# Optimization experiments

Measured on AMD Instinct MI355X. Metric: run time of the kernel, lower is better.

## Reference

```python
import jax, jax.numpy as jnp
import numpy as np

DIM = 2048
N_HEADS = 16
N_KV_HEADS = 4
HEAD_DIM = DIM // N_HEADS  # 128
N_REP = N_HEADS // N_KV_HEADS
MAX_SEQ_LEN = 4096
SEQLEN = 4096


def setup_inputs() -> dict:
    key = jax.random.key(0)
    ks = jax.random.split(key, 6)
    x = jax.random.normal(ks[0], (1, SEQLEN, DIM), dtype=jnp.float32)
    # rotary frequencies, llama-style theta=10000
    inv_freq = 1.0 / (10000.0 ** (np.arange(0, HEAD_DIM, 2, dtype=np.float32) / HEAD_DIM))
    t = np.arange(SEQLEN, dtype=np.float32)
    ang = np.outer(t, inv_freq)  # [S, head_dim/2]
    freqs_cos = jnp.asarray(np.cos(ang))
    freqs_sin = jnp.asarray(np.sin(ang))
    # additive causal mask [S, S]
    mask = jnp.where(jnp.tril(jnp.ones((SEQLEN, SEQLEN), dtype=bool)), 0.0, -1e9).astype(jnp.float32)
    sc = 0.02
    wq = jax.random.normal(ks[1], (DIM, N_HEADS * HEAD_DIM), dtype=jnp.float32) * sc
    wk = jax.random.normal(ks[2], (DIM, N_KV_HEADS * HEAD_DIM), dtype=jnp.float32) * sc
    wv = jax.random.normal(ks[3], (DIM, N_KV_HEADS * HEAD_DIM), dtype=jnp.float32) * sc
    wo = jax.random.normal(ks[4], (N_HEADS * HEAD_DIM, DIM), dtype=jnp.float32) * sc
    return {"x": x, "start_pos": 0, "freqs_cos": freqs_cos, "freqs_sin": freqs_sin,
            "mask": mask, "wq": wq, "wk": wk, "wv": wv, "wo": wo}


def _rope(x, cos, sin):
    # x: [b, s, h, d]; cos/sin: [s, d/2]; consecutive pairs form complex numbers
    b, s, h, d = x.shape
    xr = x.astype(jnp.float32).reshape(b, s, h, d // 2, 2)
    x1, x2 = xr[..., 0], xr[..., 1]
    c = cos[None, :, None, :]
    sn = sin[None, :, None, :]
    o1 = x1 * c - x2 * sn
    o2 = x1 * sn + x2 * c
    return jnp.stack([o1, o2], axis=-1).reshape(b, s, h, d).astype(x.dtype)


def reference(x, start_pos, freqs_cos, freqs_sin, mask, wq, wk, wv, wo):
    bsz, seqlen, _ = x.shape
    xq = (x @ wq).reshape(bsz, seqlen, N_HEADS, HEAD_DIM)
    xk = (x @ wk).reshape(bsz, seqlen, N_KV_HEADS, HEAD_DIM)
    xv = (x @ wv).reshape(bsz, seqlen, N_KV_HEADS, HEAD_DIM)
    xq = _rope(xq, freqs_cos, freqs_sin)
    xk = _rope(xk, freqs_cos, freqs_sin)
    # KV-cache append (cache is zeros before this call)
    cache_k = jnp.zeros((1, MAX_SEQ_LEN, N_KV_HEADS, HEAD_DIM), dtype=xk.dtype)
    cache_v = jnp.zeros((1, MAX_SEQ_LEN, N_KV_HEADS, HEAD_DIM), dtype=xv.dtype)
    cache_k = jax.lax.dynamic_update_slice(cache_k, xk, (0, start_pos, 0, 0))
    cache_v = jax.lax.dynamic_update_slice(cache_v, xv, (0, start_pos, 0, 0))
    keys = cache_k[:bsz, : start_pos + seqlen]    # [b, T, kvh, d]
    values = cache_v[:bsz, : start_pos + seqlen]
    # GQA repeat to full head count
    keys = jnp.repeat(keys, N_REP, axis=2)
    values = jnp.repeat(values, N_REP, axis=2)
    scale = 1.0 / jnp.sqrt(jnp.float32(HEAD_DIM))
    scores = jnp.einsum('bshd,bthd->bhst', xq, keys) * scale  # [b, h, s, T]
    scores = scores + mask[None, None, :, :]
    probs = jax.nn.softmax(scores.astype(jnp.float32), axis=-1).astype(xq.dtype)
    out = jnp.einsum('bhst,bthd->bshd', probs, values).reshape(bsz, seqlen, -1)
    return out @ wo
```

## Files before the change

### kernel.cpp

```cpp
#include <hip/hip_runtime.h>
#include <hip/hip_bf16.h>
#include <stdint.h>

#define SEQ 4096
#define DIM 2048
#define NH 16
#define NKV 4
#define HD 128
#define KVLD 1024


using frag8 = __attribute__((ext_vector_type(8))) short;
using f32x4 = __attribute__((ext_vector_type(4))) float;

union VecU { ushort u[8]; uint4 v; };

__device__ __forceinline__ float bf2f(ushort u) {
    union { uint32_t u; float f; } v; v.u = ((uint32_t)u) << 16; return v.f;
}
__device__ __forceinline__ ushort f2bf(float f) {
    union { float f; uint32_t u; } v; v.f = f;
    uint32_t r = v.u + 0x7fffu + ((v.u >> 16) & 1u);
    return (ushort)(r >> 16);
}

__device__ __forceinline__ void glds16(const void* g, void* l) {
    __builtin_amdgcn_global_load_lds(
        (const __attribute__((address_space(1))) void*)g,
        (__attribute__((address_space(3))) void*)l, 16, 0, 0);
}

__global__ __launch_bounds__(256) void cvt_kernel(
    const float* __restrict__ src, ushort* __restrict__ dst)
{
    size_t i = ((size_t)blockIdx.x * 256 + threadIdx.x) * 8;
    float4 f0 = *(const float4*)&src[i];
    float4 f1 = *(const float4*)&src[i + 4];
    VecU t;
    t.u[0] = f2bf(f0.x); t.u[1] = f2bf(f0.y); t.u[2] = f2bf(f0.z); t.u[3] = f2bf(f0.w);
    t.u[4] = f2bf(f1.x); t.u[5] = f2bf(f1.y); t.u[6] = f2bf(f1.z); t.u[7] = f2bf(f1.w);
    *(uint4*)&dst[i] = t.v;
}

__global__ __launch_bounds__(256) void convT_kernel(
    const float* __restrict__ src, ushort* __restrict__ dst, int K, int N)
{
    __shared__ ushort T[32][36];
    int r  = threadIdx.x >> 3;
    int c4 = (threadIdx.x & 7) * 4;
    int bk = blockIdx.y * 32, bn = blockIdx.x * 32;
    float4 v = *(const float4*)&src[(size_t)(bk + r) * N + bn + c4];
    T[r][c4]     = f2bf(v.x); T[r][c4 + 1] = f2bf(v.y);
    T[r][c4 + 2] = f2bf(v.z); T[r][c4 + 3] = f2bf(v.w);
    __syncthreads();
    ushort4 o;
    o.x = T[c4][r]; o.y = T[c4 + 1][r]; o.z = T[c4 + 2][r]; o.w = T[c4 + 3][r];
    *(ushort4*)&dst[(size_t)(bn + r) * K + bk + c4] = o;
}

__global__ __launch_bounds__(256) void vtrans_kernel(
    const ushort* __restrict__ src, ushort* __restrict__ dst)
{
    __shared__ ushort T[32][36];
    int r  = threadIdx.x >> 3;
    int c4 = (threadIdx.x & 7) * 4;
    int bt = blockIdx.y * 32, bd = blockIdx.x * 32;
    ushort4 v = *(const ushort4*)&src[(size_t)(bt + r) * KVLD + 512 + bd + c4];
    T[r][c4] = v.x; T[r][c4 + 1] = v.y; T[r][c4 + 2] = v.z; T[r][c4 + 3] = v.w;
    __syncthreads();
    ushort4 o;
    o.x = T[c4][r]; o.y = T[c4 + 1][r]; o.z = T[c4 + 2][r]; o.w = T[c4 + 3][r];
    *(ushort4*)&dst[(size_t)(bd + r) * SEQ + bt + c4] = o;
}

template <int CF>
__global__ __launch_bounds__(256) void gemm_tn(
    const ushort* __restrict__ A, const ushort* __restrict__ BT,
    void* __restrict__ C, int M, int N, int K)
{
    __shared__ ushort As[128 * 32];
    __shared__ ushort Bs[128 * 32];

    const int tid  = threadIdx.x;
    const int lane = tid & 63;
    const int wave = tid >> 6;
    const int bm   = blockIdx.y * 128;
    const int bn   = blockIdx.x * 128;
    const int wm   = (wave >> 1) * 64;
    const int wn   = (wave & 1) * 64;
    const int quad = lane >> 4;
    const int t16  = lane & 15;
    const int kg   = quad ^ ((t16 >> 1) & 3);

    f32x4 acc[4][4] = {};

    for (int k0 = 0; k0 < K; k0 += 32) {
        #pragma unroll
        for (int it = 0; it < 2; ++it) {
            int gid = it * 256 + tid;
            int r   = gid >> 2;
            int cs  = (gid & 3) ^ ((gid >> 3) & 3);
            glds16(&A[(size_t)(bm + r) * K + k0 + cs * 8],
                   &As[(it * 256 + wave * 64) * 8]);
            glds16(&BT[(size_t)(bn + r) * K + k0 + cs * 8],
                   &Bs[(it * 256 + wave * 64) * 8]);
        }
        __syncthreads();

        frag8 af[4], bf[4];
        #pragma unroll
        for (int i = 0; i < 4; ++i)
            af[i] = *(const frag8*)&As[(wm + i * 16 + t16) * 32 + kg * 8];
        #pragma unroll
        for (int j = 0; j < 4; ++j)
            bf[j] = *(const frag8*)&Bs[(wn + j * 16 + t16) * 32 + kg * 8];
        #pragma unroll
        for (int i = 0; i < 4; ++i)
            #pragma unroll
            for (int j = 0; j < 4; ++j)
                acc[i][j] = __builtin_amdgcn_mfma_f32_16x16x32_bf16(
                    af[i], bf[j], acc[i][j], 0, 0, 0);
        __syncthreads();
    }

    #pragma unroll
    for (int i = 0; i < 4; ++i)
        #pragma unroll
        for (int j = 0; j < 4; ++j)
            #pragma unroll
            for (int r = 0; r < 4; ++r) {
                int row = bm + wm + i * 16 + quad * 4 + r;
                int col = bn + wn + j * 16 + t16;
                if (CF) ((float*)C)[(size_t)row * N + col] = acc[i][j][r];
                else    ((ushort*)C)[(size_t)row * N + col] = f2bf(acc[i][j][r]);
            }
}

__global__ __launch_bounds__(256) void gemm_qkv(
    const ushort* __restrict__ A, const ushort* __restrict__ BT,
    ushort* __restrict__ Cq, ushort* __restrict__ Ckv)
{
    const int K = DIM;
    __shared__ ushort As[128 * 32];
    __shared__ ushort Bs[128 * 32];

    const int tid  = threadIdx.x;
    const int lane = tid & 63;
    const int wave = tid >> 6;
    const int bm   = blockIdx.y * 128;
    const int bn   = blockIdx.x * 128;
    const int wm   = (wave >> 1) * 64;
    const int wn   = (wave & 1) * 64;
    const int quad = lane >> 4;
    const int t16  = lane & 15;
    const int kg   = quad ^ ((t16 >> 1) & 3);

    f32x4 acc[4][4] = {};

    for (int k0 = 0; k0 < K; k0 += 32) {
        #pragma unroll
        for (int it = 0; it < 2; ++it) {
            int gid = it * 256 + tid;
            int r   = gid >> 2;
            int cs  = (gid & 3) ^ ((gid >> 3) & 3);
            glds16(&A[(size_t)(bm + r) * K + k0 + cs * 8],
                   &As[(it * 256 + wave * 64) * 8]);
            glds16(&BT[(size_t)(bn + r) * K + k0 + cs * 8],
                   &Bs[(it * 256 + wave * 64) * 8]);
        }
        __syncthreads();

        frag8 af[4], bf[4];
        #pragma unroll
        for (int i = 0; i < 4; ++i)
            af[i] = *(const frag8*)&As[(wm + i * 16 + t16) * 32 + kg * 8];
        #pragma unroll
        for (int j = 0; j < 4; ++j)
            bf[j] = *(const frag8*)&Bs[(wn + j * 16 + t16) * 32 + kg * 8];
        #pragma unroll
        for (int i = 0; i < 4; ++i)
            #pragma unroll
            for (int j = 0; j < 4; ++j)
                acc[i][j] = __builtin_amdgcn_mfma_f32_16x16x32_bf16(
                    af[i], bf[j], acc[i][j], 0, 0, 0);
        __syncthreads();
    }

    ushort* C;
    int ldc, cb;
    if (bn < 2048) { C = Cq;  ldc = DIM;  cb = 0; }
    else           { C = Ckv; ldc = KVLD; cb = 2048; }

    #pragma unroll
    for (int i = 0; i < 4; ++i)
        #pragma unroll
        for (int j = 0; j < 4; ++j)
            #pragma unroll
            for (int r = 0; r < 4; ++r) {
                int row = bm + wm + i * 16 + quad * 4 + r;
                int col = bn + wn + j * 16 + t16;
                C[(size_t)row * ldc + (col - cb)] = f2bf(acc[i][j][r]);
            }
}

__global__ void rope_kernel(ushort* __restrict__ X, const float* __restrict__ Cos,
                            const float* __restrict__ Sin, int log2nh, int strideT,
                            float oscale)
{
    int idx = blockIdx.x * blockDim.x + threadIdx.x;
    int p = idx & 63;
    int h = (idx >> 6) & ((1 << log2nh) - 1);
    int t = idx >> (6 + log2nh);
    size_t base = (size_t)t * strideT + (size_t)h * 128 + 2 * p;
    ushort2 xv = *(ushort2*)&X[base];
    float x1 = bf2f(xv.x), x2 = bf2f(xv.y);
    float c = Cos[t * 64 + p], s = Sin[t * 64 + p];
    ushort2 ov;
    ov.x = f2bf((x1 * c - x2 * s) * oscale);
    ov.y = f2bf((x1 * s + x2 * c) * oscale);
    *(ushort2*)&X[base] = ov;
}

__global__ __launch_bounds__(256) void attn_kernel(
    const ushort* __restrict__ Q, const ushort* __restrict__ Kb,
    const ushort* __restrict__ VT, ushort* __restrict__ O)
{
    __shared__ ushort Ks[64][136];
    __shared__ ushort Vt[128][72];
    __shared__ ushort Sp[4][16][72];

    const int tid  = threadIdx.x;
    const int lane = tid & 63;
    const int wave = tid >> 6;
    const int quad = lane >> 4;
    const int t16  = lane & 15;
    const int h    = blockIdx.x;
    const int kvh  = h >> 2;

    frag8 vONE;
    #pragma unroll
    for (int i = 0; i < 8; ++i) vONE[i] = (short)0x3F80;

    const int qt = 63 - (int)blockIdx.y;
    const int q0 = qt * 64;
    const int qwave = q0 + wave * 16;
    const int qmaxw = qwave + 15;

    frag8 aQ[4];
    #pragma unroll
    for (int kk = 0; kk < 4; ++kk)
        aQ[kk] = *(const frag8*)&Q[(size_t)(qwave + t16) * DIM + h * HD + kk * 32 + quad * 8];

    f32x4 o[8] = {};
    f32x4 o9 = {0.f, 0.f, 0.f, 0.f};
    float mrow[4];
    #pragma unroll
    for (int r = 0; r < 4; ++r) mrow[r] = -30000.f;

    for (int t0 = 0; t0 <= q0 + 63; t0 += 64) {
        #pragma unroll
        for (int it = 0; it < 4; ++it) {
            int idx = tid + it * 256;
            int tt  = idx >> 4;
            int c   = (idx & 15) * 8;
            *(uint4*)&Ks[tt][c] =
                *(const uint4*)&Kb[(size_t)(t0 + tt) * KVLD + kvh * HD + c];
        }
        #pragma unroll
        for (int it = 0; it < 4; ++it) {
            int idx = tid + it * 256;
            int d   = idx >> 3;
            int tq  = (idx & 7) * 8;
            *(uint4*)&Vt[d][tq] =
                *(const uint4*)&VT[(size_t)(kvh * HD + d) * SEQ + t0 + tq];
        }
        __syncthreads();

        const bool hi = (t0 + 32 <= qmaxw);
        {
            f32x4 s0 = {0.f, 0.f, 0.f, 0.f};
            f32x4 s1 = {0.f, 0.f, 0.f, 0.f};
            f32x4 s2 = {0.f, 0.f, 0.f, 0.f};
            f32x4 s3 = {0.f, 0.f, 0.f, 0.f};
            __builtin_amdgcn_s_setprio(1);
            #pragma unroll
            for (int kk = 0; kk < 4; ++kk) {
                frag8 b0 = *(const frag8*)&Ks[2 * t16][kk * 32 + quad * 8];
                frag8 b1 = *(const frag8*)&Ks[2 * t16 + 1][kk * 32 + quad * 8];
                s0 = __builtin_amdgcn_mfma_f32_16x16x32_bf16(aQ[kk], b0, s0, 0, 0, 0);
                s1 = __builtin_amdgcn_mfma_f32_16x16x32_bf16(aQ[kk], b1, s1, 0, 0, 0);
            }
            if (hi) {
                #pragma unroll
                for (int kk = 0; kk < 4; ++kk) {
                    frag8 b2 = *(const frag8*)&Ks[32 + 2 * t16][kk * 32 + quad * 8];
                    frag8 b3 = *(const frag8*)&Ks[33 + 2 * t16][kk * 32 + quad * 8];
                    s2 = __builtin_amdgcn_mfma_f32_16x16x32_bf16(aQ[kk], b2, s2, 0, 0, 0);
                    s3 = __builtin_amdgcn_mfma_f32_16x16x32_bf16(aQ[kk], b3, s3, 0, 0, 0);
                }
            }
            __builtin_amdgcn_s_setprio(0);

            const bool mLo = (t0 + 31 > qwave);
            const bool mHi = (t0 + 63 > qwave);
            float v[4][4];
            float mnew[4];
            bool trig = false;
            #pragma unroll
            for (int r = 0; r < 4; ++r) {
                int q = qwave + quad * 4 + r;
                float v0 = s0[r];
                float v1 = s1[r];
                float v2 = hi ? s2[r] : -30000.f;
                float v3 = hi ? s3[r] : -30000.f;
                if (mLo) {
                    if (t0 + 2 * t16 > q)      v0 = -30000.f;
                    if (t0 + 2 * t16 + 1 > q)  v1 = -30000.f;
                }
                if (hi && mHi) {
                    if (t0 + 32 + 2 * t16 > q) v2 = -30000.f;
                    if (t0 + 33 + 2 * t16 > q) v3 = -30000.f;
                }
                float rm = fmaxf(fmaxf(v0, v1), fmaxf(v2, v3));
                rm = fmaxf(rm, __shfl_xor(rm, 1));
                rm = fmaxf(rm, __shfl_xor(rm, 2));
                rm = fmaxf(rm, __shfl_xor(rm, 4));
                rm = fmaxf(rm, __shfl_xor(rm, 8));
                mnew[r] = fmaxf(mrow[r], rm);
                trig |= (rm > mrow[r] + 8.f);
                v[r][0] = v0; v[r][1] = v1; v[r][2] = v2; v[r][3] = v3;
            }
            if (__any(trig)) {
                #pragma unroll
                for (int r = 0; r < 4; ++r) {
                    float alpha = __expf(mrow[r] - mnew[r]);
                    mrow[r] = mnew[r];
                    #pragma unroll
                    for (int j = 0; j < 8; ++j) o[j][r] *= alpha;
                    o9[r] *= alpha;
                }
            }
            #pragma unroll
            for (int r = 0; r < 4; ++r) {
                float e0 = __expf(v[r][0] - mrow[r]);
                float e1 = __expf(v[r][1] - mrow[r]);
                uint pv = (uint)f2bf(e0) | ((uint)f2bf(e1) << 16);
                *(uint*)&Sp[wave][quad * 4 + r][2 * t16] = pv;
                if (hi) {
                    float e2 = __expf(v[r][2] - mrow[r]);
                    float e3 = __expf(v[r][3] - mrow[r]);
                    uint ph = (uint)f2bf(e2) | ((uint)f2bf(e3) << 16);
                    *(uint*)&Sp[wave][quad * 4 + r][32 + 2 * t16] = ph;
                }
            }

            frag8 aP0 = *(const frag8*)&Sp[wave][t16][quad * 8];
            __builtin_amdgcn_s_setprio(1);
            #pragma unroll
            for (int j = 0; j < 8; ++j) {
                frag8 bV = *(const frag8*)&Vt[j * 16 + t16][quad * 8];
                o[j] = __builtin_amdgcn_mfma_f32_16x16x32_bf16(aP0, bV, o[j], 0, 0, 0);
            }
            o9 = __builtin_amdgcn_mfma_f32_16x16x32_bf16(aP0, vONE, o9, 0, 0, 0);
            if (hi) {
                frag8 aP1 = *(const frag8*)&Sp[wave][t16][32 + quad * 8];
                #pragma unroll
                for (int j = 0; j < 8; ++j) {
                    frag8 bV = *(const frag8*)&Vt[j * 16 + t16][32 + quad * 8];
                    o[j] = __builtin_amdgcn_mfma_f32_16x16x32_bf16(aP1, bV, o[j], 0, 0, 0);
                }
                o9 = __builtin_amdgcn_mfma_f32_16x16x32_bf16(aP1, vONE, o9, 0, 0, 0);
            }
            __builtin_amdgcn_s_setprio(0);
        }
        __syncthreads();
    }

    #pragma unroll
    for (int r = 0; r < 4; ++r) {
        float inv = 1.f / fmaxf(o9[r], 1e-20f);
        int row = qwave + quad * 4 + r;
        #pragma unroll
        for (int j = 0; j < 8; ++j)
            O[(size_t)row * DIM + h * HD + j * 16 + t16] = f2bf(o[j][r] * inv);
    }
}

extern "C" void kernel_launch(void* const* d_in, const int* in_sizes, int n_in,
                              void* d_out, int out_size, void* d_ws, size_t ws_size,
                              hipStream_t stream)
{
    const float* x  = (const float*)d_in[0];
    const float* fc = (const float*)d_in[2];
    const float* fs = (const float*)d_in[3];
    const float* wq = (const float*)d_in[5];
    const float* wk = (const float*)d_in[6];
    const float* wv = (const float*)d_in[7];
    const float* wo = (const float*)d_in[8];

    ushort* Qb  = (ushort*)d_ws;
    ushort* KVb = Qb + (size_t)SEQ * DIM;
    ushort* Ab  = KVb + (size_t)SEQ * KVLD;
    ushort* WqT = Ab;
    ushort* KVT = Ab + (size_t)DIM * DIM;
    ushort* WoT = KVb;

    ushort* Xb = (ushort*)d_out;
    ushort* VT = Xb + (size_t)SEQ * DIM;

    dim3 blk(256);

    cvt_kernel<<<(SEQ * DIM) / 2048, blk, 0, stream>>>(x, Xb);
    convT_kernel<<<dim3(DIM / 32, DIM / 32), blk, 0, stream>>>(wq, WqT, DIM, DIM);
    convT_kernel<<<dim3(512 / 32, DIM / 32), blk, 0, stream>>>(wk, KVT, DIM, 512);
    convT_kernel<<<dim3(512 / 32, DIM / 32), blk, 0, stream>>>(
        wv, KVT + (size_t)512 * DIM, DIM, 512);

    gemm_qkv<<<dim3(3072 / 128, SEQ / 128), blk, 0, stream>>>(Xb, Ab, Qb, KVb);

    rope_kernel<<<(SEQ * NH * 64) / 256, blk, 0, stream>>>(
        Qb, fc, fs, 4, DIM, 0.08838834764831845f);
    rope_kernel<<<(SEQ * NKV * 64) / 256, blk, 0, stream>>>(
        KVb, fc, fs, 2, KVLD, 1.0f);

    vtrans_kernel<<<dim3(512 / 32, SEQ / 32), blk, 0, stream>>>(KVb, VT);

    attn_kernel<<<dim3(NH, 64), blk, 0, stream>>>(Qb, KVb, VT, Ab);

    convT_kernel<<<dim3(DIM / 32, DIM / 32), blk, 0, stream>>>(wo, WoT, DIM, DIM);
    gemm_tn<1><<<dim3(DIM / 128, SEQ / 128), blk, 0, stream>>>(Ab, WoT, d_out, SEQ, DIM, DIM);
}
```

Baseline: 452.8 us.

## Process two query heads per attention block to reuse K/V tiles

Each attention workgroup now handles two query heads that share one KV head, so every K and V tile staged in shared memory serves twice the MFMA work and the grid is halved. The softmax is restructured to compute exponentials optimistically against the previous running max and to recompute only when a row max rises by more than a threshold. The running max now starts at zero instead of a large negative value. Launch bounds request two blocks per CU. The cost is roughly doubled accumulator and Q-fragment registers, which may cause spills or lower occupancy, and fewer blocks to spread across the CUs.

```diff
diff --git a/kernel.cpp b/kernel.cpp
--- a/kernel.cpp
+++ b/kernel.cpp
@@ -221,21 +221,23 @@
     *(ushort2*)&X[base] = ov;
 }
 
-__global__ __launch_bounds__(256) void attn_kernel(
+__global__ __launch_bounds__(256, 2) void attn_kernel(
     const ushort* __restrict__ Q, const ushort* __restrict__ Kb,
     const ushort* __restrict__ VT, ushort* __restrict__ O)
 {
     __shared__ ushort Ks[64][136];
     __shared__ ushort Vt[128][72];
-    __shared__ ushort Sp[4][16][72];
+    __shared__ ushort Sp[4][32][72];
 
     const int tid  = threadIdx.x;
     const int lane = tid & 63;
     const int wave = tid >> 6;
     const int quad = lane >> 4;
     const int t16  = lane & 15;
-    const int h    = blockIdx.x;
-    const int kvh  = h >> 2;
+    const int hp   = blockIdx.x;
+    const int hA   = 2 * hp;
+    const int hB   = 2 * hp + 1;
+    const int kvh  = hp >> 1;
 
     frag8 vONE;
     #pragma unroll
@@ -246,16 +248,18 @@
     const int qwave = q0 + wave * 16;
     const int qmaxw = qwave + 15;
 
-    frag8 aQ[4];
+    frag8 aQA[4], aQB[4];
     #pragma unroll
-    for (int kk = 0; kk < 4; ++kk)
-        aQ[kk] = *(const frag8*)&Q[(size_t)(qwave + t16) * DIM + h * HD + kk * 32 + quad * 8];
-
-    f32x4 o[8] = {};
-    f32x4 o9 = {0.f, 0.f, 0.f, 0.f};
-    float mrow[4];
-    #pragma unroll
-    for (int r = 0; r < 4; ++r) mrow[r] = -30000.f;
+    for (int kk = 0; kk < 4; ++kk) {
+        aQA[kk] = *(const frag8*)&Q[(size_t)(qwave + t16) * DIM + hA * HD + kk * 32 + quad * 8];
+        aQB[kk] = *(const frag8*)&Q[(size_t)(qwave + t16) * DIM + hB * HD + kk * 32 + quad * 8];
+    }
+
+    f32x4 oA[8] = {}, oB[8] = {};
+    f32x4 o9A = {0.f, 0.f, 0.f, 0.f};
+    f32x4 o9B = {0.f, 0.f, 0.f, 0.f};
+    float mA[4] = {0.f, 0.f, 0.f, 0.f};
+    float mB[4] = {0.f, 0.f, 0.f, 0.f};
 
     for (int t0 = 0; t0 <= q0 + 63; t0 += 64) {
         #pragma unroll
@@ -277,112 +281,169 @@
         __syncthreads();
 
         const bool hi = (t0 + 32 <= qmaxw);
-        {
-            f32x4 s0 = {0.f, 0.f, 0.f, 0.f};
-            f32x4 s1 = {0.f, 0.f, 0.f, 0.f};
-            f32x4 s2 = {0.f, 0.f, 0.f, 0.f};
-            f32x4 s3 = {0.f, 0.f, 0.f, 0.f};
-            __builtin_amdgcn_s_setprio(1);
+
+        f32x4 sA0 = {0.f,0.f,0.f,0.f}, sA1 = {0.f,0.f,0.f,0.f};
+        f32x4 sA2 = {0.f,0.f,0.f,0.f}, sA3 = {0.f,0.f,0.f,0.f};
+        f32x4 sB0 = {0.f,0.f,0.f,0.f}, sB1 = {0.f,0.f,0.f,0.f};
+        f32x4 sB2 = {0.f,0.f,0.f,0.f}, sB3 = {0.f,0.f,0.f,0.f};
+
+        __builtin_amdgcn_s_setprio(1);
+        #pragma unroll
+        for (int kk = 0; kk < 4; ++kk) {
+            frag8 b0 = *(const frag8*)&Ks[2 * t16][kk * 32 + quad * 8];
+            frag8 b1 = *(const frag8*)&Ks[2 * t16 + 1][kk * 32 + quad * 8];
+            sA0 = __builtin_amdgcn_mfma_f32_16x16x32_bf16(aQA[kk], b0, sA0, 0, 0, 0);
+            sB0 = __builtin_amdgcn_mfma_f32_16x16x32_bf16(aQB[kk], b0, sB0, 0, 0, 0);
+            sA1 = __builtin_amdgcn_mfma_f32_16x16x32_bf16(aQA[kk], b1, sA1, 0, 0, 0);
+            sB1 = __builtin_amdgcn_mfma_f32_16x16x32_bf16(aQB[kk], b1, sB1, 0, 0, 0);
+        }
+        if (hi) {
             #pragma unroll
             for (int kk = 0; kk < 4; ++kk) {
-                frag8 b0 = *(const frag8*)&Ks[2 * t16][kk * 32 + quad * 8];
-                frag8 b1 = *(const frag8*)&Ks[2 * t16 + 1][kk * 32 + quad * 8];
-                s0 = __builtin_amdgcn_mfma_f32_16x16x32_bf16(aQ[kk], b0, s0, 0, 0, 0);
-                s1 = __builtin_amdgcn_mfma_f32_16x16x32_bf16(aQ[kk], b1, s1, 0, 0, 0);
-            }
+                frag8 b2 = *(const frag8*)&Ks[32 + 2 * t16][kk * 32 + quad * 8];
+                frag8 b3 = *(const frag8*)&Ks[33 + 2 * t16][kk * 32 + quad * 8];
+                sA2 = __builtin_amdgcn_mfma_f32_16x16x32_bf16(aQA[kk], b2, sA2, 0, 0, 0);
+                sB2 = __builtin_amdgcn_mfma_f32_16x16x32_bf16(aQB[kk], b2, sB2, 0, 0, 0);
+                sA3 = __builtin_amdgcn_mfma_f32_16x16x32_bf16(aQA[kk], b3, sA3, 0, 0, 0);
+                sB3 = __builtin_amdgcn_mfma_f32_16x16x32_bf16(aQB[kk], b3, sB3, 0, 0, 0);
+            }
+        }
+        __builtin_amdgcn_s_setprio(0);
+
+        const bool mLo = (t0 + 31 > qwave);
+        const bool mHi = (t0 + 63 > qwave);
+
+        bool trig = false;
+        #pragma unroll
+        for (int r = 0; r < 4; ++r) {
+            int q = qwave + quad * 4 + r;
+            bool x0 = mLo && (t0 + 2 * t16 > q);
+            bool x1 = mLo && (t0 + 2 * t16 + 1 > q);
+            bool x2 = mHi && (t0 + 32 + 2 * t16 > q);
+            bool x3 = mHi && (t0 + 33 + 2 * t16 > q);
+            float vA0 = x0 ? -30000.f : sA0[r];
+            float vA1 = x1 ? -30000.f : sA1[r];
+            float vA2 = (hi && !x2) ? sA2[r] : -30000.f;
+            float vA3 = (hi && !x3) ? sA3[r] : -30000.f;
+            float vB0 = x0 ? -30000.f : sB0[r];
+            float vB1 = x1 ? -30000.f : sB1[r];
+            float vB2 = (hi && !x2) ? sB2[r] : -30000.f;
+            float vB3 = (hi && !x3) ? sB3[r] : -30000.f;
+            float lmA = fmaxf(fmaxf(vA0, vA1), fmaxf(vA2, vA3));
+            float lmB = fmaxf(fmaxf(vB0, vB1), fmaxf(vB2, vB3));
+            trig |= (lmA > mA[r] + 8.f) | (lmB > mB[r] + 8.f);
+            float eA0 = __expf(vA0 - mA[r]);
+            float eA1 = __expf(vA1 - mA[r]);
+            float eB0 = __expf(vB0 - mB[r]);
+            float eB1 = __expf(vB1 - mB[r]);
+            *(uint*)&Sp[wave][quad * 4 + r][2 * t16] =
+                (uint)f2bf(eA0) | ((uint)f2bf(eA1) << 16);
+            *(uint*)&Sp[wave][16 + quad * 4 + r][2 * t16] =
+                (uint)f2bf(eB0) | ((uint)f2bf(eB1) << 16);
             if (hi) {
-                #pragma unroll
-                for (int kk = 0; kk < 4; ++kk) {
-                    frag8 b2 = *(const frag8*)&Ks[32 + 2 * t16][kk * 32 + quad * 8];
-                    frag8 b3 = *(const frag8*)&Ks[33 + 2 * t16][kk * 32 + quad * 8];
-                    s2 = __builtin_amdgcn_mfma_f32_16x16x32_bf16(aQ[kk], b2, s2, 0, 0, 0);
-                    s3 = __builtin_amdgcn_mfma_f32_16x16x32_bf16(aQ[kk], b3, s3, 0, 0, 0);
-                }
-            }
-            __builtin_amdgcn_s_setprio(0);
-
-            const bool mLo = (t0 + 31 > qwave);
-            const bool mHi = (t0 + 63 > qwave);
-            float v[4][4];
-            float mnew[4];
-            bool trig = false;
+                float eA2 = __expf(vA2 - mA[r]);
+                float eA3 = __expf(vA3 - mA[r]);
+                float eB2 = __expf(vB2 - mB[r]);
+                float eB3 = __expf(vB3 - mB[r]);
+                *(uint*)&Sp[wave][quad * 4 + r][32 + 2 * t16] =
+                    (uint)f2bf(eA2) | ((uint)f2bf(eA3) << 16);
+                *(uint*)&Sp[wave][16 + quad * 4 + r][32 + 2 * t16] =
+                    (uint)f2bf(eB2) | ((uint)f2bf(eB3) << 16);
+            }
+        }
+
+        if (__any(trig)) {
             #pragma unroll
             for (int r = 0; r < 4; ++r) {
                 int q = qwave + quad * 4 + r;
-                float v0 = s0[r];
-                float v1 = s1[r];
-                float v2 = hi ? s2[r] : -30000.f;
-                float v3 = hi ? s3[r] : -30000.f;
-                if (mLo) {
-                    if (t0 + 2 * t16 > q)      v0 = -30000.f;
-                    if (t0 + 2 * t16 + 1 > q)  v1 = -30000.f;
+                bool x0 = mLo && (t0 + 2 * t16 > q);
+                bool x1 = mLo && (t0 + 2 * t16 + 1 > q);
+                bool x2 = mHi && (t0 + 32 + 2 * t16 > q);
+                bool x3 = mHi && (t0 + 33 + 2 * t16 > q);
+                float vA0 = x0 ? -30000.f : sA0[r];
+                float vA1 = x1 ? -30000.f : sA1[r];
+                float vA2 = (hi && !x2) ? sA2[r] : -30000.f;
+                float vA3 = (hi && !x3) ? sA3[r] : -30000.f;
+                float vB0 = x0 ? -30000.f : sB0[r];
+                float vB1 = x1 ? -30000.f : sB1[r];
+                float vB2 = (hi && !x2) ? sB2[r] : -30000.f;
+                float vB3 = (hi && !x3) ? sB3[r] : -30000.f;
+                float rmA = fmaxf(fmaxf(vA0, vA1), fmaxf(vA2, vA3));
+                float rmB = fmaxf(fmaxf(vB0, vB1), fmaxf(vB2, vB3));
+                rmA = fmaxf(rmA, __shfl_xor(rmA, 1));
+                rmA = fmaxf(rmA, __shfl_xor(rmA, 2));
+                rmA = fmaxf(rmA, __shfl_xor(rmA, 4));
+                rmA = fmaxf(rmA, __shfl_xor(rmA, 8));
+                rmB = fmaxf(rmB, __shfl_xor(rmB, 1));
+                rmB = fmaxf(rmB, __shfl_xor(rmB, 2));
+                rmB = fmaxf(rmB, __shfl_xor(rmB, 4));
+                rmB = fmaxf(rmB, __shfl_xor(rmB, 8));
+                float mnA = fmaxf(mA[r], rmA);
+                float mnB = fmaxf(mB[r], rmB);
+                float alA = __expf(mA[r] - mnA);
+                float alB = __expf(mB[r] - mnB);
+                #pragma unroll
+                for (int j = 0; j < 8; ++j) { oA[j][r] *= alA; oB[j][r] *= alB; }
+                o9A[r] *= alA; o9B[r] *= alB;
+                mA[r] = mnA; mB[r] = mnB;
+                float eA0 = __expf(vA0 - mnA);
+                float eA1 = __expf(vA1 - mnA);
+                float eB0 = __expf(vB0 - mnB);
+                float eB1 = __expf(vB1 - mnB);
+                *(uint*)&Sp[wave][quad * 4 + r][2 * t16] =
+                    (uint)f2bf(eA0) | ((uint)f2bf(eA1) << 16);
+                *(uint*)&Sp[wave][16 + quad * 4 + r][2 * t16] =
+                    (uint)f2bf(eB0) | ((uint)f2bf(eB1) << 16);
+                if (hi) {
+                    float eA2 = __expf(vA2 - mnA);
+                    float eA3 = __expf(vA3 - mnA);
+                    float eB2 = __expf(vB2 - mnB);
+                    float eB3 = __expf(vB3 - mnB);
+                    *(uint*)&Sp[wave][quad * 4 + r][32 + 2 * t16] =
+                        (uint)f2bf(eA2) | ((uint)f2bf(eA3) << 16);
+                    *(uint*)&Sp[wave][16 + quad * 4 + r][32 + 2 * t16] =
+                        (uint)f2bf(eB2) | ((uint)f2bf(eB3) << 16);
                 }
-                if (hi && mHi) {
-                    if (t0 + 32 + 2 * t16 > q) v2 = -30000.f;
-                    if (t0 + 33 + 2 * t16 > q) v3 = -30000.f;
-                }
-                float rm = fmaxf(fmaxf(v0, v1), fmaxf(v2, v3));
-                rm = fmaxf(rm, __shfl_xor(rm, 1));
-                rm = fmaxf(rm, __shfl_xor(rm, 2));
-                rm = fmaxf(rm, __shfl_xor(rm, 4));
-                rm = fmaxf(rm, __shfl_xor(rm, 8));
-                mnew[r] = fmaxf(mrow[r], rm);
-                trig |= (rm > mrow[r] + 8.f);
-                v[r][0] = v0; v[r][1] = v1; v[r][2] = v2; v[r][3] = v3;
-            }
-            if (__any(trig)) {
-                #pragma unroll
-                for (int r = 0; r < 4; ++r) {
-                    float alpha = __expf(mrow[r] - mnew[r]);
-                    mrow[r] = mnew[r];
-                    #pragma unroll
-                    for (int j = 0; j < 8; ++j) o[j][r] *= alpha;
-                    o9[r] *= alpha;
-                }
-            }
-            #pragma unroll
-            for (int r = 0; r < 4; ++r) {
-                float e0 = __expf(v[r][0] - mrow[r]);
-                float e1 = __expf(v[r][1] - mrow[r]);
-                uint pv = (uint)f2bf(e0) | ((uint)f2bf(e1) << 16);
-                *(uint*)&Sp[wave][quad * 4 + r][2 * t16] = pv;
-                if (hi) {
-                    float e2 = __expf(v[r][2] - mrow[r]);
-                    float e3 = __expf(v[r][3] - mrow[r]);
-                    uint ph = (uint)f2bf(e2) | ((uint)f2bf(e3) << 16);
-                    *(uint*)&Sp[wave][quad * 4 + r][32 + 2 * t16] = ph;
-                }
-            }
-
-            frag8 aP0 = *(const frag8*)&Sp[wave][t16][quad * 8];
-            __builtin_amdgcn_s_setprio(1);
+            }
+        }
+
+        frag8 aPA0 = *(const frag8*)&Sp[wave][t16][quad * 8];
+        frag8 aPB0 = *(const frag8*)&Sp[wave][16 + t16][quad * 8];
+        __builtin_amdgcn_s_setprio(1);
+        #pragma unroll
+        for (int j = 0; j < 8; ++j) {
+            frag8 bV = *(const frag8*)&Vt[j * 16 + t16][quad * 8];
+            oA[j] = __builtin_amdgcn_mfma_f32_16x16x32_bf16(aPA0, bV, oA[j], 0, 0, 0);
+            oB[j] = __builtin_amdgcn_mfma_f32_16x16x32_bf16(aPB0, bV, oB[j], 0, 0, 0);
+        }
+        o9A = __builtin_amdgcn_mfma_f32_16x16x32_bf16(aPA0, vONE, o9A, 0, 0, 0);
+        o9B = __builtin_amdgcn_mfma_f32_16x16x32_bf16(aPB0, vONE, o9B, 0, 0, 0);
+        if (hi) {
+            frag8 aPA1 = *(const frag8*)&Sp[wave][t16][32 + quad * 8];
+            frag8 aPB1 = *(const frag8*)&Sp[wave][16 + t16][32 + quad * 8];
             #pragma unroll
             for (int j = 0; j < 8; ++j) {
-                frag8 bV = *(const frag8*)&Vt[j * 16 + t16][quad * 8];
-                o[j] = __builtin_amdgcn_mfma_f32_16x16x32_bf16(aP0, bV, o[j], 0, 0, 0);
-            }
-            o9 = __builtin_amdgcn_mfma_f32_16x16x32_bf16(aP0, vONE, o9, 0, 0, 0);
-            if (hi) {
-                frag8 aP1 = *(const frag8*)&Sp[wave][t16][32 + quad * 8];
-                #pragma unroll
-                for (int j = 0; j < 8; ++j) {
-                    frag8 bV = *(const frag8*)&Vt[j * 16 + t16][32 + quad * 8];
-                    o[j] = __builtin_amdgcn_mfma_f32_16x16x32_bf16(aP1, bV, o[j], 0, 0, 0);
-                }
-                o9 = __builtin_amdgcn_mfma_f32_16x16x32_bf16(aP1, vONE, o9, 0, 0, 0);
-            }
-            __builtin_amdgcn_s_setprio(0);
-        }
+                frag8 bV = *(const frag8*)&Vt[j * 16 + t16][32 + quad * 8];
+                oA[j] = __builtin_amdgcn_mfma_f32_16x16x32_bf16(aPA1, bV, oA[j], 0, 0, 0);
+                oB[j] = __builtin_amdgcn_mfma_f32_16x16x32_bf16(aPB1, bV, oB[j], 0, 0, 0);
+            }
+            o9A = __builtin_amdgcn_mfma_f32_16x16x32_bf16(aPA1, vONE, o9A, 0, 0, 0);
+            o9B = __builtin_amdgcn_mfma_f32_16x16x32_bf16(aPB1, vONE, o9B, 0, 0, 0);
+        }
+        __builtin_amdgcn_s_setprio(0);
         __syncthreads();
     }
 
     #pragma unroll
     for (int r = 0; r < 4; ++r) {
-        float inv = 1.f / fmaxf(o9[r], 1e-20f);
+        float invA = 1.f / fmaxf(o9A[r], 1e-20f);
+        float invB = 1.f / fmaxf(o9B[r], 1e-20f);
         int row = qwave + quad * 4 + r;
         #pragma unroll
-        for (int j = 0; j < 8; ++j)
-            O[(size_t)row * DIM + h * HD + j * 16 + t16] = f2bf(o[j][r] * inv);
+        for (int j = 0; j < 8; ++j) {
+            O[(size_t)row * DIM + hA * HD + j * 16 + t16] = f2bf(oA[j][r] * invA);
+            O[(size_t)row * DIM + hB * HD + j * 16 + t16] = f2bf(oB[j][r] * invB);
+        }
     }
 }
 
@@ -425,7 +486,7 @@
 
     vtrans_kernel<<<dim3(512 / 32, SEQ / 32), blk, 0, stream>>>(KVb, VT);
 
-    attn_kernel<<<dim3(NH, 64), blk, 0, stream>>>(Qb, KVb, VT, Ab);
+    attn_kernel<<<dim3(NH / 2, 64), blk, 0, stream>>>(Qb, KVb, VT, Ab);
 
     convT_kernel<<<dim3(DIM / 32, DIM / 32), blk, 0, stream>>>(wo, WoT, DIM, DIM);
     gemm_tn<1><<<dim3(DIM / 128, SEQ / 128), blk, 0, stream>>>(Ab, WoT, d_out, SEQ, DIM, DIM);
```

New measurement: 450.9 us. About the same (-0.4%).
